# Kernel tuning notes

Measured on AMD Instinct MI355X. Metric: run time of the kernel, lower is better.

The kernel has to match this reference:

```python
import jax, jax.numpy as jnp
import numpy as np

N_NODES = 50000
IN_CH = 128
HID_CH = 256
N_EDGES = 800000

def setup_inputs() -> dict:
    key = jax.random.key(0)
    k1, k2, k3, k4, k5 = jax.random.split(key, 5)
    x = jax.random.normal(k1, (N_NODES, IN_CH), dtype=jnp.float32)
    edge_index = jax.random.randint(k2, (2, N_EDGES), 0, N_NODES, dtype=jnp.int64)
    # SAGEConv params: lin_l (applied to aggregated neighbors, has bias), lin_r (applied to root, no bias)
    s = 1.0 / np.sqrt(IN_CH)
    W_l = jax.random.uniform(k3, (IN_CH, HID_CH), dtype=jnp.float32, minval=-s, maxval=s)
    b_l = jnp.zeros((HID_CH,), dtype=jnp.float32)
    W_r = jax.random.uniform(k4, (IN_CH, HID_CH), dtype=jnp.float32, minval=-s, maxval=s)
    return {"x": x, "edge_index": edge_index, "W_l": W_l, "b_l": b_l, "W_r": W_r}

def reference(x, edge_index, W_l, b_l, W_r):
    src, dst = edge_index[0], edge_index[1]
    # gather source features along edges, scatter-mean into destination nodes
    msgs = x[src]  # [E, in]
    agg_sum = jax.ops.segment_sum(msgs, dst, num_segments=N_NODES)  # [N, in]
    deg = jax.ops.segment_sum(jnp.ones((N_EDGES,), x.dtype), dst, num_segments=N_NODES)
    agg = agg_sum / jnp.maximum(deg, 1.0)[:, None]
    # SAGEConv: lin_l(aggregated) + lin_r(root), then ReLU
    out = agg @ W_l + b_l + x @ W_r
    return jax.nn.relu(out)
```

## Files before the change

kernel.cpp:

```cpp
#include <hip/hip_runtime.h>
#include <hip/hip_bf16.h>

#define IN_CH   128
#define HID_CH  256
#define KTOT    256
#define LDS_RS  72

#define BUCK_NODES 128
#define NBUCK      391
#define BUCK_CAP   2432

typedef __attribute__((ext_vector_type(8))) short bf16x8;
typedef __attribute__((ext_vector_type(4))) float f32x4;
typedef __attribute__((ext_vector_type(2))) float f32x2;

static __device__ __forceinline__ unsigned short f2bf(float f) {
    unsigned int u = __float_as_uint(f);
    unsigned int r = (u + 0x7FFFu + ((u >> 16) & 1u)) >> 16;
    return (unsigned short)r;
}
static __device__ __forceinline__ float bf2f(unsigned int ubits16) {
    return __uint_as_float(ubits16 << 16);
}

static __device__ __forceinline__ unsigned enc_e4m3(float f) {
    unsigned u = __float_as_uint(f);
    unsigned s = (u >> 24) & 0x80u;
    float af = fabsf(f);
    if (af >= 448.f) return s | 0x7Eu;
    if (af < 0.0009765625f) return s;
    if (af < 0.015625f) {
        int m = (int)(af * 512.0f + 0.5f);
        if (m > 7) return s | 0x08u;
        return s | (unsigned)m;
    }
    unsigned au = u & 0x7fffffffu;
    unsigned r = au + 0x0007FFFFu + ((au >> 20) & 1u);
    unsigned e8 = r >> 23;
    unsigned m = (r >> 20) & 7u;
    int e4 = (int)e8 - 120;
    if (e4 >= 16) return s | 0x7Eu;
    return s | ((unsigned)e4 << 3) | m;
}

static __device__ __forceinline__ void dec4_e4m3(unsigned v, float& c0, float& c1,
                                                 float& c2, float& c3) {
#if __has_builtin(__builtin_amdgcn_cvt_pk_f32_fp8)
    f32x2 dlo = __builtin_amdgcn_cvt_pk_f32_fp8(v, false);
    f32x2 dhi = __builtin_amdgcn_cvt_pk_f32_fp8(v, true);
    c0 = dlo.x; c1 = dlo.y; c2 = dhi.x; c3 = dhi.y;
#else
    unsigned b[4] = {v & 0xFFu, (v >> 8) & 0xFFu, (v >> 16) & 0xFFu, v >> 24};
    float o[4];
    #pragma unroll
    for (int i = 0; i < 4; ++i) {
        unsigned e = (b[i] >> 3) & 15u, m = b[i] & 7u;
        unsigned nz = (e != 0u) ? 1u : 0u;
        float val = (float)(m + (nz << 3)) * __uint_as_float((e + 117u + (1u - nz)) << 23);
        o[i] = (b[i] & 0x80u) ? -val : val;
    }
    c0 = o[0]; c1 = o[1]; c2 = o[2]; c3 = o[3];
#endif
}

__global__ __launch_bounds__(1024) void front_kernel(
    const float* __restrict__ x, const int* __restrict__ ei,
    const float* __restrict__ Wl, const float* __restrict__ Wr,
    unsigned short* __restrict__ featb, unsigned char* __restrict__ fx8,
    unsigned short* __restrict__ WT, int* __restrict__ histg,
    int N, int Npad, int E, int nchunk, int nxb)
{
    __shared__ int h[NBUCK];
    const int b = blockIdx.x, tid = threadIdx.x;

    if (b < 64) {
        int t = b * 1024 + tid;
        int n = t >> 8, k = t & 255;
        float v = (k < IN_CH) ? Wl[(size_t)k * HID_CH + n]
                              : Wr[(size_t)(k - IN_CH) * HID_CH + n];
        WT[(size_t)n * KTOT + k] = f2bf(v);
        return;
    }
    if (b < 64 + nxb) {
        int t = (b - 64) * 1024 + tid;
        if (t >= Npad * 16) return;
        int n = t >> 4, c8 = (t & 15) * 8;
        if (n >= N) {
            uint4 z = {0u, 0u, 0u, 0u};
            *reinterpret_cast<uint4*>(featb + (size_t)n * KTOT + c8) = z;
            *reinterpret_cast<uint4*>(featb + (size_t)n * KTOT + IN_CH + c8) = z;
            uint2 z2 = {0u, 0u};
            *reinterpret_cast<uint2*>(fx8 + (size_t)n * IN_CH + c8) = z2;
            return;
        }
        const float* src = x + (size_t)n * IN_CH + c8;
        float4 v0 = *reinterpret_cast<const float4*>(src);
        float4 v1 = *reinterpret_cast<const float4*>(src + 4);
        uint4 o;
        o.x = (unsigned)f2bf(v0.x) | ((unsigned)f2bf(v0.y) << 16);
        o.y = (unsigned)f2bf(v0.z) | ((unsigned)f2bf(v0.w) << 16);
        o.z = (unsigned)f2bf(v1.x) | ((unsigned)f2bf(v1.y) << 16);
        o.w = (unsigned)f2bf(v1.z) | ((unsigned)f2bf(v1.w) << 16);
        *reinterpret_cast<uint4*>(featb + (size_t)n * KTOT + IN_CH + c8) = o;
        uint2 p;
        p.x = enc_e4m3(v0.x) | (enc_e4m3(v0.y) << 8) |
              (enc_e4m3(v0.z) << 16) | (enc_e4m3(v0.w) << 24);
        p.y = enc_e4m3(v1.x) | (enc_e4m3(v1.y) << 8) |
              (enc_e4m3(v1.z) << 16) | (enc_e4m3(v1.w) << 24);
        *reinterpret_cast<uint2*>(fx8 + (size_t)n * IN_CH + c8) = p;
        return;
    }
    int c = b - 64 - nxb;
    if (tid < NBUCK) h[tid] = 0;
    __syncthreads();
    int i = c * 1024 + tid;
    if (i < E) atomicAdd(&h[((unsigned)ei[E + i]) >> 7], 1);
    __syncthreads();
    if (tid < NBUCK) histg[(size_t)tid * nchunk + c] = h[tid];
}

__global__ __launch_bounds__(1024) void rowscan_kernel(
    int* __restrict__ histg, int* __restrict__ btot, int nchunk)
{
    __shared__ int s[1024];
    const int b = blockIdx.x, t = threadIdx.x;
    int v = (t < nchunk) ? histg[(size_t)b * nchunk + t] : 0;
    s[t] = v;
    __syncthreads();
    #pragma unroll
    for (int off = 1; off < 1024; off <<= 1) {
        int add = (t >= off) ? s[t - off] : 0;
        __syncthreads();
        s[t] += add;
        __syncthreads();
    }
    if (t < nchunk) histg[(size_t)b * nchunk + t] = s[t] - v;
    if (t == 1023) btot[b] = s[1023];
}

__global__ __launch_bounds__(1024) void scatter_part_kernel(
    const int* __restrict__ ei, const int* __restrict__ histg,
    const int* __restrict__ btot, unsigned* __restrict__ barr,
    int E, int nchunk)
{
    __shared__ int cur[NBUCK];
    __shared__ int sb[512];
    const int c = blockIdx.x, t = threadIdx.x;
    if (t < 512) sb[t] = (t < NBUCK) ? btot[t] : 0;
    __syncthreads();
    #pragma unroll
    for (int off = 1; off < 512; off <<= 1) {
        int add = (t < 512 && t >= off) ? sb[t - off] : 0;
        __syncthreads();
        if (t < 512) sb[t] += add;
        __syncthreads();
    }
    if (t < NBUCK) cur[t] = histg[(size_t)t * nchunk + c] + ((t == 0) ? 0 : sb[t - 1]);
    __syncthreads();
    int i = c * 1024 + t;
    if (i < E) {
        unsigned src = (unsigned)ei[i];
        unsigned dst = (unsigned)ei[E + i];
        int pos = atomicAdd(&cur[dst >> 7], 1);
        barr[pos] = src | ((dst & 127u) << 16);
    }
}

__global__ __launch_bounds__(1024) void fused_gather_kernel(
    const unsigned* __restrict__ barr, const int* __restrict__ btot,
    const unsigned char* __restrict__ fx8, unsigned short* __restrict__ featb,
    int N)
{
    __shared__ unsigned s_edge[BUCK_CAP];
    __shared__ unsigned short s_col[BUCK_CAP];
    __shared__ int s_cnt[BUCK_NODES];
    __shared__ int s_start[BUCK_NODES];
    __shared__ int s_cur[BUCK_NODES];
    __shared__ int s_scan[BUCK_NODES];
    __shared__ int sb[512];

    const int b = blockIdx.x;
    const int tid = threadIdx.x;
    const int node0 = b * BUCK_NODES;
    const int nnodes = min(BUCK_NODES, N - node0);

    if (tid < 512) sb[tid] = (tid < NBUCK) ? btot[tid] : 0;
    if (tid < BUCK_NODES) s_cnt[tid] = 0;
    __syncthreads();
    #pragma unroll
    for (int off = 1; off < 512; off <<= 1) {
        int add = (tid < 512 && tid >= off) ? sb[tid - off] : 0;
        __syncthreads();
        if (tid < 512) sb[tid] += add;
        __syncthreads();
    }
    const int base = (b == 0) ? 0 : sb[b - 1];
    int nb = btot[b];
    nb = (nb < BUCK_CAP) ? nb : BUCK_CAP;

    for (int i = tid; i < nb; i += 1024) {
        unsigned p = barr[(size_t)base + i];
        s_edge[i] = p;
        atomicAdd(&s_cnt[p >> 16], 1);
    }
    __syncthreads();

    if (tid < BUCK_NODES) s_scan[tid] = s_cnt[tid];
    __syncthreads();
    #pragma unroll
    for (int off = 1; off < BUCK_NODES; off <<= 1) {
        int add = 0;
        if (tid < BUCK_NODES && tid >= off) add = s_scan[tid - off];
        __syncthreads();
        if (tid < BUCK_NODES) s_scan[tid] += add;
        __syncthreads();
    }
    if (tid < BUCK_NODES) {
        int st = s_scan[tid] - s_cnt[tid];
        s_start[tid] = st;
        s_cur[tid] = st;
    }
    __syncthreads();

    for (int i = tid; i < nb; i += 1024) {
        unsigned p = s_edge[i];
        int pos = atomicAdd(&s_cur[p >> 16], 1);
        s_col[pos] = (unsigned short)(p & 0xFFFFu);
    }
    __syncthreads();

    const int wid = tid >> 6, lane = tid & 63;
    const int half = lane >> 5, sub = lane & 31;
    for (int pr = wid; pr < BUCK_NODES / 2; pr += 16) {
        int ln = pr * 2 + half;
        bool live = (ln < nnodes);
        int deg = live ? s_cnt[ln] : 0;
        int beg = live ? s_start[ln] : 0;
        float a0 = 0.f, a1 = 0.f, a2 = 0.f, a3 = 0.f;
        for (int e = 0; e < deg; e += 8) {
            unsigned vv[8];
            #pragma unroll
            for (int q = 0; q < 8; ++q) {
                int ee = e + q;
                ee = (ee < deg) ? ee : (deg - 1);
                int s = s_col[beg + ee];
                vv[q] = *reinterpret_cast<const unsigned*>(
                    fx8 + (size_t)s * IN_CH + sub * 4);
            }
            #pragma unroll
            for (int q = 0; q < 8; ++q) {
                float m = (e + q < deg) ? 1.f : 0.f;
                float c0, c1, c2, c3;
                dec4_e4m3(vv[q], c0, c1, c2, c3);
                a0 = fmaf(m, c0, a0); a1 = fmaf(m, c1, a1);
                a2 = fmaf(m, c2, a2); a3 = fmaf(m, c3, a3);
            }
        }
        if (live) {
            float inv = 1.0f / fmaxf((float)deg, 1.0f);
            uint2 o;
            o.x = (unsigned)f2bf(a0 * inv) | ((unsigned)f2bf(a1 * inv) << 16);
            o.y = (unsigned)f2bf(a2 * inv) | ((unsigned)f2bf(a3 * inv) << 16);
            *reinterpret_cast<uint2*>(
                featb + (size_t)(node0 + ln) * KTOT + sub * 4) = o;
        }
    }
}

__global__ __launch_bounds__(256, 2) void sage_mfma_kernel(
    const unsigned short* __restrict__ featb,
    const unsigned short* __restrict__ WT,
    const float* __restrict__ bl,
    float* __restrict__ out, int N)
{
    __shared__ unsigned short sA[128][LDS_RS];
    __shared__ unsigned short sB[256][LDS_RS];

    const int tid   = threadIdx.x;
    const int nbase = blockIdx.x * 128;
    const int lane  = tid & 63;
    const int w     = tid >> 6;
    const int wr    = (w >> 1) * 64;
    const int wc    = (w & 1) * 128;
    const int lr    = lane & 15;
    const int lk    = (lane >> 4) * 8;

    f32x4 acc[4][8] = {};

    for (int kb = 0; kb < KTOT; kb += 64) {
        __syncthreads();
        #pragma unroll
        for (int p = 0; p < 4; ++p) {
            int c = tid + p * 256;
            int row = c >> 3, q = c & 7;
            uint4 va = *reinterpret_cast<const uint4*>(
                featb + (size_t)(nbase + row) * KTOT + kb + q * 8);
            *reinterpret_cast<uint4*>(&sA[row][q * 8]) = va;
        }
        #pragma unroll
        for (int p = 0; p < 8; ++p) {
            int c = tid + p * 256;
            int row = c >> 3, q = c & 7;
            uint4 vb = *reinterpret_cast<const uint4*>(
                WT + (size_t)row * KTOT + kb + q * 8);
            *reinterpret_cast<uint4*>(&sB[row][q * 8]) = vb;
        }
        __syncthreads();
        #pragma unroll
        for (int ks = 0; ks < 2; ++ks) {
            bf16x8 af[4], bfr[8];
            #pragma unroll
            for (int i = 0; i < 4; ++i)
                af[i] = *reinterpret_cast<const bf16x8*>(&sA[wr + i * 16 + lr][ks * 32 + lk]);
            #pragma unroll
            for (int i = 0; i < 8; ++i)
                bfr[i] = *reinterpret_cast<const bf16x8*>(&sB[wc + i * 16 + lr][ks * 32 + lk]);
            #pragma unroll
            for (int mi = 0; mi < 4; ++mi)
                #pragma unroll
                for (int ni = 0; ni < 8; ++ni)
                    acc[mi][ni] = __builtin_amdgcn_mfma_f32_16x16x32_bf16(
                        af[mi], bfr[ni], acc[mi][ni], 0, 0, 0);
        }
    }

    #pragma unroll
    for (int ni = 0; ni < 8; ++ni) {
        float bias = bl[wc + ni * 16 + lr];
        #pragma unroll
        for (int mi = 0; mi < 4; ++mi) {
            #pragma unroll
            for (int r = 0; r < 4; ++r) {
                int row = nbase + wr + mi * 16 + (lane >> 4) * 4 + r;
                if (row < N) {
                    int colj = wc + ni * 16 + lr;
                    out[(size_t)row * HID_CH + colj] = fmaxf(acc[mi][ni][r] + bias, 0.0f);
                }
            }
        }
    }
}

extern "C" void kernel_launch(void* const* d_in, const int* in_sizes, int n_in,
                              void* d_out, int out_size, void* d_ws, size_t ws_size,
                              hipStream_t stream) {
    const float* x  = (const float*)d_in[0];
    const int*   ei = (const int*)d_in[1];
    const float* Wl = (const float*)d_in[2];
    const float* bl = (const float*)d_in[3];
    const float* Wr = (const float*)d_in[4];
    float* out = (float*)d_out;

    const int N = in_sizes[0] / IN_CH;
    const int E = in_sizes[1] / 2;
    const int Npad   = ((N + 127) / 128) * 128;
    const int nchunk = (E + 1023) / 1024;
    const int nxb    = (Npad * 16 + 1023) / 1024;

    unsigned short* featb = (unsigned short*)d_ws;
    unsigned short* WT    = featb + (size_t)Npad * KTOT;
    unsigned char*  fx8   = (unsigned char*)(WT + KTOT * HID_CH);
    unsigned* barr = (unsigned*)(fx8 + (size_t)Npad * IN_CH);
    int* histg = (int*)(barr + E);
    int* btot  = histg + (size_t)NBUCK * nchunk;

    front_kernel<<<64 + nxb + nchunk, 1024, 0, stream>>>(
        x, ei, Wl, Wr, featb, fx8, WT, histg, N, Npad, E, nchunk, nxb);
    rowscan_kernel<<<NBUCK, 1024, 0, stream>>>(histg, btot, nchunk);
    scatter_part_kernel<<<nchunk, 1024, 0, stream>>>(ei, histg, btot, barr, E, nchunk);
    fused_gather_kernel<<<NBUCK, 1024, 0, stream>>>(barr, btot, fx8, featb, N);
    sage_mfma_kernel<<<Npad / 128, 256, 0, stream>>>(featb, WT, bl, out, N);
}
```

Baseline: 87.37 us.

## Stage edge partition in LDS and enlarge chunks for coalesced bucket writes

After: 82.84 us. 1.05x faster.

```diff
diff --git a/kernel.cpp b/kernel.cpp
--- a/kernel.cpp
+++ b/kernel.cpp
@@ -9,6 +9,7 @@
 #define BUCK_NODES 128
 #define NBUCK      391
 #define BUCK_CAP   2432
+#define SCHUNK     4096
 
 typedef __attribute__((ext_vector_type(8))) short bf16x8;
 typedef __attribute__((ext_vector_type(4))) float f32x4;
@@ -113,8 +114,11 @@
     int c = b - 64 - nxb;
     if (tid < NBUCK) h[tid] = 0;
     __syncthreads();
-    int i = c * 1024 + tid;
-    if (i < E) atomicAdd(&h[((unsigned)ei[E + i]) >> 7], 1);
+    #pragma unroll
+    for (int r = 0; r < SCHUNK / 1024; ++r) {
+        int i = c * SCHUNK + r * 1024 + tid;
+        if (i < E) atomicAdd(&h[((unsigned)ei[E + i]) >> 7], 1);
+    }
     __syncthreads();
     if (tid < NBUCK) histg[(size_t)tid * nchunk + c] = h[tid];
 }
@@ -143,26 +147,82 @@
     const int* __restrict__ btot, unsigned* __restrict__ barr,
     int E, int nchunk)
 {
-    __shared__ int cur[NBUCK];
+    __shared__ unsigned stagr[SCHUNK];
+    __shared__ unsigned stag[SCHUNK];
+    __shared__ unsigned short bidr[SCHUNK];
+    __shared__ unsigned short bid[SCHUNK];
+    __shared__ int lh[NBUCK];
+    __shared__ int lstart[NBUCK];
+    __shared__ int lc[NBUCK];
+    __shared__ int ls[512];
     __shared__ int sb[512];
-    const int c = blockIdx.x, t = threadIdx.x;
-    if (t < 512) sb[t] = (t < NBUCK) ? btot[t] : 0;
+
+    const int c = blockIdx.x, tid = threadIdx.x;
+    const int e0 = c * SCHUNK;
+    const int nval = min(SCHUNK, E - e0);
+
+    if (tid < NBUCK) lh[tid] = 0;
+    if (tid < 512) sb[tid] = (tid < NBUCK) ? btot[tid] : 0;
+    __syncthreads();
+
+    #pragma unroll
+    for (int r = 0; r < SCHUNK / 1024; ++r) {
+        int li = r * 1024 + tid;
+        if (li < nval) {
+            int i = e0 + li;
+            unsigned src = (unsigned)ei[i];
+            unsigned dst = (unsigned)ei[E + i];
+            unsigned bkt = dst >> 7;
+            stagr[li] = src | ((dst & 127u) << 16);
+            bidr[li] = (unsigned short)bkt;
+            atomicAdd(&lh[bkt], 1);
+        }
+    }
     __syncthreads();
     #pragma unroll
     for (int off = 1; off < 512; off <<= 1) {
-        int add = (t < 512 && t >= off) ? sb[t - off] : 0;
-        __syncthreads();
-        if (t < 512) sb[t] += add;
-        __syncthreads();
-    }
-    if (t < NBUCK) cur[t] = histg[(size_t)t * nchunk + c] + ((t == 0) ? 0 : sb[t - 1]);
-    __syncthreads();
-    int i = c * 1024 + t;
-    if (i < E) {
-        unsigned src = (unsigned)ei[i];
-        unsigned dst = (unsigned)ei[E + i];
-        int pos = atomicAdd(&cur[dst >> 7], 1);
-        barr[pos] = src | ((dst & 127u) << 16);
+        int add = (tid < 512 && tid >= off) ? sb[tid - off] : 0;
+        __syncthreads();
+        if (tid < 512) sb[tid] += add;
+        __syncthreads();
+    }
+    if (tid < 512) ls[tid] = (tid < NBUCK) ? lh[tid] : 0;
+    __syncthreads();
+    #pragma unroll
+    for (int off = 1; off < 512; off <<= 1) {
+        int add = (tid < 512 && tid >= off) ? ls[tid - off] : 0;
+        __syncthreads();
+        if (tid < 512) ls[tid] += add;
+        __syncthreads();
+    }
+    if (tid < NBUCK) {
+        int st = ls[tid] - lh[tid];
+        lstart[tid] = st;
+        lc[tid] = 0;
+    }
+    __syncthreads();
+
+    #pragma unroll
+    for (int r = 0; r < SCHUNK / 1024; ++r) {
+        int li = r * 1024 + tid;
+        if (li < nval) {
+            unsigned bkt = bidr[li];
+            int pos = lstart[bkt] + atomicAdd(&lc[bkt], 1);
+            stag[pos] = stagr[li];
+            bid[pos] = (unsigned short)bkt;
+        }
+    }
+    __syncthreads();
+
+    #pragma unroll
+    for (int r = 0; r < SCHUNK / 1024; ++r) {
+        int li = r * 1024 + tid;
+        if (li < nval) {
+            unsigned bkt = bid[li];
+            int gbase = histg[(size_t)bkt * nchunk + c] +
+                        ((bkt == 0) ? 0 : sb[bkt - 1]);
+            barr[(size_t)gbase + (li - lstart[bkt])] = stag[li];
+        }
     }
 }
 
@@ -354,7 +414,7 @@
     const int N = in_sizes[0] / IN_CH;
     const int E = in_sizes[1] / 2;
     const int Npad   = ((N + 127) / 128) * 128;
-    const int nchunk = (E + 1023) / 1024;
+    const int nchunk = (E + SCHUNK - 1) / SCHUNK;
     const int nxb    = (Npad * 16 + 1023) / 1024;
 
     unsigned short* featb = (unsigned short*)d_ws;
```
